# Kernel optimization log

Hardware: AMD Instinct MI355X
Metric: run time of the kernel (lower is better)

The kernel has to match this reference:

```python
import jax, jax.numpy as jnp
import numpy as np

EPS = 1e-12


def setup_inputs() -> dict:
    key = jax.random.key(0)
    k1, k2, k3 = jax.random.split(key, 3)
    N, D, K = 131072, 64, 1024
    input_data = jax.random.normal(k1, (N, D), dtype=jnp.float32)
    codebooks = jax.random.normal(k2, (K, D), dtype=jnp.float32)
    random_vector = jax.random.normal(k3, (N, D), dtype=jnp.float32)
    return {"input_data": input_data, "codebooks": codebooks, "random_vector": random_vector}


def reference(input_data, codebooks, random_vector):
    # input_data: (N, D); codebooks: (K, D); random_vector: (N, D)
    N = input_data.shape[0]
    K = codebooks.shape[0]

    distances = (
        jnp.sum(input_data ** 2, axis=1, keepdims=True)
        - 2.0 * (input_data @ codebooks.T)
        + jnp.sum(codebooks ** 2, axis=1)[None, :]
    )
    min_indices = jnp.argmin(distances, axis=1)  # (N,)
    hard_quantized_input = codebooks[min_indices]  # (N, D) gather

    # Noise-substitution VQ: replace residual with a random vector of equal norm
    norm_residual = jnp.sqrt(jnp.sum((input_data - hard_quantized_input) ** 2, axis=1, keepdims=True))
    norm_random = jnp.sqrt(jnp.sum(random_vector ** 2, axis=1, keepdims=True))
    vq_error = (norm_residual / (norm_random + EPS)) * random_vector
    quantized_input = input_data + vq_error

    # Usage counts via scatter-add (equivalent to one-hot encodings mean)
    counts = jnp.zeros((K,), dtype=jnp.int32).at[min_indices].add(1)
    avg_probs = counts.astype(jnp.float32) / jnp.float32(N)
    perplexity = jnp.exp(-jnp.sum(avg_probs * jnp.log(avg_probs + EPS)))

    codebooks_used = counts  # torch module accumulates; fresh buffer starts at zero
    return quantized_input, perplexity, codebooks_used
```

## Files before the change

### kernel.cpp

```cpp
#include <hip/hip_runtime.h>
#include <math.h>


#define NSVQ_D 64
#define ABN 512
#define THR_Q 12u

typedef __attribute__((ext_vector_type(8))) _Float16 half8;
typedef __attribute__((ext_vector_type(16))) float f32x16;

__global__ __launch_bounds__(256)
void nsvq_prep(const float* __restrict__ cb,
               ushort* __restrict__ cbf,
               float* __restrict__ cn2k, int* __restrict__ counts, int K) {
  if (blockIdx.x == 0) ((int4*)counts)[threadIdx.x] = make_int4(0, 0, 0, 0);
  int r = blockIdx.x * 256 + threadIdx.x;
  if (r >= K) return;
  const float* row = cb + (long)r * NSVQ_D;
  float nrm = 0.f;
#pragma unroll
  for (int j = 0; j < 8; ++j) {
    float4 v0 = *(const float4*)(row + j * 8);
    float4 v1 = *(const float4*)(row + j * 8 + 4);
    float f[8] = {v0.x, v0.y, v0.z, v0.w, v1.x, v1.y, v1.z, v1.w};
    half8 hv;
#pragma unroll
    for (int e = 0; e < 8; ++e) {
      nrm = fmaf(f[e], f[e], nrm);
      hv[e] = (_Float16)f[e];
    }
    int blk = (r >> 5) * 256 + (j >> 1) * 64 + (j & 1) * 32 + (r & 31);
    *(half8*)(cbf + blk * 8) = hv;
  }
  cn2k[r] = 2048.f * (nrm + 512.f);
}

__global__ __launch_bounds__(1024, 1)
void nsvq_fused(const float* __restrict__ x,
                const ushort* __restrict__ cbf,
                const float* __restrict__ cn2k,
                const float* __restrict__ cb,
                const float* __restrict__ rv,
                int* __restrict__ counts,
                float* __restrict__ out) {
  __shared__ ushort CS[65536];
  __shared__ float CN[1024];
  __shared__ uint bestLds[ABN];
  __shared__ int hist[1024];

  const int tid = threadIdx.x;
  const int lane = tid & 63;
  const int wid = tid >> 6;
  const int l31 = lane & 31;
  const int lh = lane >> 5;
  const long brow = (long)blockIdx.x * ABN;
  const int wrow = wid * 32;

#pragma unroll
  for (int i = 0; i < 8; ++i) {
    int e = i * 1024 + tid;
    ((uint4*)CS)[e] = ((const uint4*)cbf)[e];
  }
  CN[tid] = cn2k[tid];
  hist[tid] = 0;

  half8 ax[4];
#pragma unroll
  for (int ks = 0; ks < 4; ++ks) {
    const float* xr = x + (brow + wrow + l31) * NSVQ_D + ks * 16 + lh * 8;
    float4 v0 = *(const float4*)xr;
    float4 v1 = *(const float4*)(xr + 4);
    float f[8] = {v0.x, v0.y, v0.z, v0.w, v1.x, v1.y, v1.z, v1.w};
    half8 h;
#pragma unroll
    for (int j = 0; j < 8; ++j) h[j] = (_Float16)(f[j] * -4096.f);
    ax[ks] = h;
  }

  uint u1[16], u2[16];
#pragma unroll
  for (int i = 0; i < 16; ++i) { u1[i] = 0xFFFFFFFFu; u2[i] = 0xFFFFFFFFu; }

  __syncthreads();

  auto LOADL = [&](half8 (&B)[4], float& cn, int g) {
    const ushort* p = CS + (g * 256 + lane) * 8;
#pragma unroll
    for (int ks = 0; ks < 4; ++ks) B[ks] = *(const half8*)(p + ks * 512);
    cn = CN[g * 32 + l31];
  };
  auto COMPUTE = [&](const half8 (&B)[4], float cc, int g) {
    const uint kidx = (uint)(g * 32 + l31);
    f32x16 a = {cc, cc, cc, cc, cc, cc, cc, cc, cc, cc, cc, cc, cc, cc, cc, cc};
    a = __builtin_amdgcn_mfma_f32_32x32x16_f16(ax[0], B[0], a, 0, 0, 0);
    a = __builtin_amdgcn_mfma_f32_32x32x16_f16(ax[1], B[1], a, 0, 0, 0);
    a = __builtin_amdgcn_mfma_f32_32x32x16_f16(ax[2], B[2], a, 0, 0, 0);
    a = __builtin_amdgcn_mfma_f32_32x32x16_f16(ax[3], B[3], a, 0, 0, 0);
#pragma unroll
    for (int r = 0; r < 16; ++r) {
      uint m = (__float_as_uint(a[r]) & 0xFFFFFC00u) | kidx;
      uint mm;
      asm("v_med3_u32 %0, %1, %2, %3" : "=v"(mm)
          : "v"(u1[r]), "v"(u2[r]), "v"(m));
      u2[r] = mm;
      u1[r] = min(u1[r], m);
    }
  };

  half8 BA[4], BB[4];
  float cnA, cnB;
  LOADL(BA, cnA, 0);
  LOADL(BB, cnB, 1);

  for (int g = 0; g < 32; g += 2) {
    COMPUTE(BA, cnA, g);
    LOADL(BA, cnA, (g + 2) & 31);
    COMPUTE(BB, cnB, g + 1);
    LOADL(BB, cnB, (g + 3) & 31);
  }

#pragma unroll
  for (int r = 0; r < 16; ++r) {
    uint a1 = u1[r], a2 = u2[r];
#pragma unroll
    for (int off = 1; off < 32; off <<= 1) {
      uint o1 = (uint)__shfl_xor((int)a1, off);
      uint o2 = (uint)__shfl_xor((int)a2, off);
      a2 = min(min(a2, o2), max(a1, o1));
      a1 = min(a1, o1);
    }
    if (l31 == 0) {
      int rowloc = (r & 3) + 8 * (r >> 2) + 4 * lh;
      bool fl = (a2 >> 10) - (a1 >> 10) < THR_Q;
      bestLds[wrow + rowloc] =
          fl ? (0x80000000u | ((a2 & 1023u) << 10) | (a1 & 1023u)) : a1;
    }
  }
  __syncthreads();

  const int l = tid & 15;
  const int rbase = tid >> 4;
#pragma unroll
  for (int pass = 0; pass < 8; ++pass) {
    const int rloc = pass * 64 + rbase;
    const long row = brow + rloc;
    uint p = bestLds[rloc];
    uint k = p & 1023u;
    float4 xv = ((const float4*)(x + row * NSVQ_D))[l];
    float sraw;

    if (p & 0x80000000u) {
      uint k2 = (p >> 10) & 1023u;
      float4 a = ((const float4*)(cb + (long)k * NSVQ_D))[l];
      float4 b = ((const float4*)(cb + (long)k2 * NSVQ_D))[l];
      float d1 = xv.x * a.x + xv.y * a.y + xv.z * a.z + xv.w * a.w;
      float d2 = xv.x * b.x + xv.y * b.y + xv.z * b.z + xv.w * b.w;
#pragma unroll
      for (int off = 1; off < 16; off <<= 1) {
        d1 += __shfl_xor(d1, off, 64);
        d2 += __shfl_xor(d2, off, 64);
      }
      float s1 = fmaf(-4096.f, d1, cn2k[k]);
      float s2 = fmaf(-4096.f, d2, cn2k[k2]);
      if (s2 < s1 || (s2 == s1 && k2 < k)) { k = k2; s1 = s2; }
      sraw = s1;
    } else {
      sraw = __uint_as_float(p & 0xFFFFFC00u);
    }

    float4 rr = ((const float4*)(rv + row * NSVQ_D))[l];
    float xx = xv.x * xv.x + xv.y * xv.y + xv.z * xv.z + xv.w * xv.w;
    float drnd = rr.x * rr.x + rr.y * rr.y + rr.z * rr.z + rr.w * rr.w;
#pragma unroll
    for (int off = 1; off < 16; off <<= 1) {
      xx += __shfl_xor(xx, off, 64);
      drnd += __shfl_xor(drnd, off, 64);
    }
    float dres = fmaxf(fmaf(sraw, 1.f / 2048.f, xx - 512.f), 0.f);
    float scale = sqrtf(dres) / (sqrtf(drnd) + 1e-12f);

    float4 o;
    o.x = xv.x + scale * rr.x;
    o.y = xv.y + scale * rr.y;
    o.z = xv.z + scale * rr.z;
    o.w = xv.w + scale * rr.w;
    ((float4*)(out + row * NSVQ_D))[l] = o;

    if (l == 0) atomicAdd(&hist[k], 1);
  }

  __syncthreads();
  int v = hist[tid];
  if (v) atomicAdd(&counts[tid], v);
}

__global__ void nsvq_perp_kernel(const int* __restrict__ counts,
                                 float* __restrict__ out_tail,
                                 float invN, int K) {
  int t = threadIdx.x;
  float v = 0.f;
  if (t < K) {
    int c = counts[t];
    out_tail[1 + t] = (float)c;
    float p = (float)c * invN;
    v = p * logf(p + 1e-12f);
  }
#pragma unroll
  for (int off = 1; off < 64; off <<= 1) v += __shfl_xor(v, off, 64);
  __shared__ float red[16];
  int wid = t >> 6;
  if ((t & 63) == 0) red[wid] = v;
  __syncthreads();
  if (t == 0) {
    float s = 0.f;
    int nw = (blockDim.x + 63) / 64;
    for (int w = 0; w < nw; ++w) s += red[w];
    out_tail[0] = expf(-s);
  }
}

extern "C" void kernel_launch(void* const* d_in, const int* in_sizes, int n_in,
                              void* d_out, int out_size, void* d_ws, size_t ws_size,
                              hipStream_t stream) {
  const float* x  = (const float*)d_in[0];
  const float* cb = (const float*)d_in[1];
  const float* rv = (const float*)d_in[2];
  float* out = (float*)d_out;

  const int D = NSVQ_D;
  const int N = in_sizes[0] / D;
  const int K = in_sizes[1] / D;

  float*  cn2k   = (float*)d_ws;
  int*    counts = (int*)((char*)d_ws + 4096);
  ushort* cbf    = (ushort*)((char*)d_ws + 8192);

  nsvq_prep<<<(K + 255) / 256, 256, 0, stream>>>(cb, cbf, cn2k, counts, K);
  nsvq_fused<<<N / ABN, 1024, 0, stream>>>(x, cbf, cn2k, cb, rv, counts, out);
  nsvq_perp_kernel<<<1, 1024, 0, stream>>>(counts, out + (size_t)N * D, 1.0f / (float)N, K);
}
```

Before: 61.16 us.

## Keep x rows in registers and run epilogue per wave without block sync

The fp32 input rows loaded for the MFMA A-operand are kept in registers, and ||x||^2 is computed at load time. The epilogue is remapped so each wave handles its own 32 rows, two lanes per row, with no block barrier and no second global read of x. The codebook norm lookup now reads LDS instead of global memory. In exchange, register pressure rises (x and rv held as float4 arrays), and the rv and output accesses become strided per lane (a lane covers 32 bytes per 64-byte k-slice), which may coalesce less well than the earlier 16-lanes-per-row layout.

```diff
diff --git a/kernel.cpp b/kernel.cpp
--- a/kernel.cpp
+++ b/kernel.cpp
@@ -65,15 +65,23 @@
   hist[tid] = 0;
 
   half8 ax[4];
+  float4 xf[8];
+  float xxloc = 0.f;
+  const long grow = brow + wrow + l31;
 #pragma unroll
   for (int ks = 0; ks < 4; ++ks) {
-    const float* xr = x + (brow + wrow + l31) * NSVQ_D + ks * 16 + lh * 8;
+    const float* xr = x + grow * NSVQ_D + ks * 16 + lh * 8;
     float4 v0 = *(const float4*)xr;
     float4 v1 = *(const float4*)(xr + 4);
-    float f[8] = {v0.x, v0.y, v0.z, v0.w, v1.x, v1.y, v1.z, v1.w};
+    xf[ks * 2] = v0;
+    xf[ks * 2 + 1] = v1;
+    xxloc += v0.x * v0.x + v0.y * v0.y + v0.z * v0.z + v0.w * v0.w;
+    xxloc += v1.x * v1.x + v1.y * v1.y + v1.z * v1.z + v1.w * v1.w;
     half8 h;
-#pragma unroll
-    for (int j = 0; j < 8; ++j) h[j] = (_Float16)(f[j] * -4096.f);
+    h[0] = (_Float16)(v0.x * -4096.f); h[1] = (_Float16)(v0.y * -4096.f);
+    h[2] = (_Float16)(v0.z * -4096.f); h[3] = (_Float16)(v0.w * -4096.f);
+    h[4] = (_Float16)(v1.x * -4096.f); h[5] = (_Float16)(v1.y * -4096.f);
+    h[6] = (_Float16)(v1.z * -4096.f); h[7] = (_Float16)(v1.w * -4096.f);
     ax[ks] = h;
   }
 
@@ -136,58 +144,66 @@
           fl ? (0x80000000u | ((a2 & 1023u) << 10) | (a1 & 1023u)) : a1;
     }
   }
-  __syncthreads();
-
-  const int l = tid & 15;
-  const int rbase = tid >> 4;
-#pragma unroll
-  for (int pass = 0; pass < 8; ++pass) {
-    const int rloc = pass * 64 + rbase;
-    const long row = brow + rloc;
-    uint p = bestLds[rloc];
-    uint k = p & 1023u;
-    float4 xv = ((const float4*)(x + row * NSVQ_D))[l];
-    float sraw;
-
-    if (p & 0x80000000u) {
-      uint k2 = (p >> 10) & 1023u;
-      float4 a = ((const float4*)(cb + (long)k * NSVQ_D))[l];
-      float4 b = ((const float4*)(cb + (long)k2 * NSVQ_D))[l];
-      float d1 = xv.x * a.x + xv.y * a.y + xv.z * a.z + xv.w * a.w;
-      float d2 = xv.x * b.x + xv.y * b.y + xv.z * b.z + xv.w * b.w;
-#pragma unroll
-      for (int off = 1; off < 16; off <<= 1) {
-        d1 += __shfl_xor(d1, off, 64);
-        d2 += __shfl_xor(d2, off, 64);
-      }
-      float s1 = fmaf(-4096.f, d1, cn2k[k]);
-      float s2 = fmaf(-4096.f, d2, cn2k[k2]);
-      if (s2 < s1 || (s2 == s1 && k2 < k)) { k = k2; s1 = s2; }
-      sraw = s1;
-    } else {
-      sraw = __uint_as_float(p & 0xFFFFFC00u);
-    }
-
-    float4 rr = ((const float4*)(rv + row * NSVQ_D))[l];
-    float xx = xv.x * xv.x + xv.y * xv.y + xv.z * xv.z + xv.w * xv.w;
-    float drnd = rr.x * rr.x + rr.y * rr.y + rr.z * rr.z + rr.w * rr.w;
-#pragma unroll
-    for (int off = 1; off < 16; off <<= 1) {
-      xx += __shfl_xor(xx, off, 64);
-      drnd += __shfl_xor(drnd, off, 64);
-    }
-    float dres = fmaxf(fmaf(sraw, 1.f / 2048.f, xx - 512.f), 0.f);
-    float scale = sqrtf(dres) / (sqrtf(drnd) + 1e-12f);
-
-    float4 o;
-    o.x = xv.x + scale * rr.x;
-    o.y = xv.y + scale * rr.y;
-    o.z = xv.z + scale * rr.z;
-    o.w = xv.w + scale * rr.w;
-    ((float4*)(out + row * NSVQ_D))[l] = o;
-
-    if (l == 0) atomicAdd(&hist[k], 1);
-  }
+
+  uint p = bestLds[wrow + l31];
+  uint k = p & 1023u;
+  float sraw;
+  if (p & 0x80000000u) {
+    uint k2 = (p >> 10) & 1023u;
+    float d1 = 0.f, d2 = 0.f;
+#pragma unroll
+    for (int ks = 0; ks < 4; ++ks) {
+      const float* c1p = cb + (long)k * NSVQ_D + ks * 16 + lh * 8;
+      const float* c2p = cb + (long)k2 * NSVQ_D + ks * 16 + lh * 8;
+      float4 a0 = *(const float4*)c1p, a1v = *(const float4*)(c1p + 4);
+      float4 b0 = *(const float4*)c2p, b1v = *(const float4*)(c2p + 4);
+      float4 x0 = xf[ks * 2], x1 = xf[ks * 2 + 1];
+      d1 += x0.x * a0.x + x0.y * a0.y + x0.z * a0.z + x0.w * a0.w;
+      d1 += x1.x * a1v.x + x1.y * a1v.y + x1.z * a1v.z + x1.w * a1v.w;
+      d2 += x0.x * b0.x + x0.y * b0.y + x0.z * b0.z + x0.w * b0.w;
+      d2 += x1.x * b1v.x + x1.y * b1v.y + x1.z * b1v.z + x1.w * b1v.w;
+    }
+    d1 += __shfl_xor(d1, 32, 64);
+    d2 += __shfl_xor(d2, 32, 64);
+    float s1 = fmaf(-4096.f, d1, CN[k]);
+    float s2 = fmaf(-4096.f, d2, CN[k2]);
+    if (s2 < s1 || (s2 == s1 && k2 < k)) { k = k2; s1 = s2; }
+    sraw = s1;
+  } else {
+    sraw = __uint_as_float(p & 0xFFFFFC00u);
+  }
+
+  float4 rr[8];
+  float drnd = 0.f;
+#pragma unroll
+  for (int ks = 0; ks < 4; ++ks) {
+    const float* rp = rv + grow * NSVQ_D + ks * 16 + lh * 8;
+    float4 r0 = *(const float4*)rp;
+    float4 r1 = *(const float4*)(rp + 4);
+    rr[ks * 2] = r0;
+    rr[ks * 2 + 1] = r1;
+    drnd += r0.x * r0.x + r0.y * r0.y + r0.z * r0.z + r0.w * r0.w;
+    drnd += r1.x * r1.x + r1.y * r1.y + r1.z * r1.z + r1.w * r1.w;
+  }
+  float xx = xxloc + __shfl_xor(xxloc, 32, 64);
+  drnd += __shfl_xor(drnd, 32, 64);
+  float dres = fmaxf(fmaf(sraw, 1.f / 2048.f, xx - 512.f), 0.f);
+  float scale = sqrtf(dres) / (sqrtf(drnd) + 1e-12f);
+
+#pragma unroll
+  for (int ks = 0; ks < 4; ++ks) {
+    float* op = out + grow * NSVQ_D + ks * 16 + lh * 8;
+    float4 x0 = xf[ks * 2], x1 = xf[ks * 2 + 1];
+    float4 r0 = rr[ks * 2], r1 = rr[ks * 2 + 1];
+    float4 o0, o1;
+    o0.x = x0.x + scale * r0.x; o0.y = x0.y + scale * r0.y;
+    o0.z = x0.z + scale * r0.z; o0.w = x0.w + scale * r0.w;
+    o1.x = x1.x + scale * r1.x; o1.y = x1.y + scale * r1.y;
+    o1.z = x1.z + scale * r1.z; o1.w = x1.w + scale * r1.w;
+    *(float4*)op = o0;
+    *(float4*)(op + 4) = o1;
+  }
+  if (lh == 0) atomicAdd(&hist[k], 1);
 
   __syncthreads();
   int v = hist[tid];
```

Result: faster. 57.58 us (-5.9%).
